# Performance work log

Measured on AMD Instinct MI355X. Metric: run time of the kernel, lower is better.

Reference implementation:

```python
import jax, jax.numpy as jnp
import numpy as np

HEAD_DIM = 128
ROPE_THETA = 10000.0


def _rope_cos_sin(positions, head_dim, theta):
    # positions: [T] int -> cos/sin [T, head_dim] (LLaMA half-split convention)
    inv_freq = 1.0 / (theta ** (jnp.arange(0, head_dim, 2, dtype=jnp.float32) / head_dim))
    ang = positions.astype(jnp.float32)[:, None] * inv_freq  # [T, D/2]
    cos = jnp.concatenate([jnp.cos(ang), jnp.cos(ang)], axis=-1)
    sin = jnp.concatenate([jnp.sin(ang), jnp.sin(ang)], axis=-1)
    return cos, sin


def _apply_rope(x, cos, sin):
    # x: [T, H, D]; rotate_half: (-x2, x1)
    half = x.shape[-1] // 2
    rot = jnp.concatenate([-x[..., half:], x[..., :half]], axis=-1)
    return x * cos[:, None, :] + rot * sin[:, None, :]


def setup_inputs() -> dict:
    key = jax.random.key(0)
    ks = jax.random.split(key, 5)
    T, hid = 4096, 4096
    S = 1024  # equal-length sequences -> B = T // S = 4
    Hq, Hk, D = 32, 8, HEAD_DIM
    hidden = jax.random.normal(ks[0], (T, hid), dtype=jnp.float32)
    positions = (jnp.arange(T, dtype=jnp.int32) % S)
    q_w = jax.random.normal(ks[1], (Hq * D, hid), dtype=jnp.float32) * 0.02
    k_w = jax.random.normal(ks[2], (Hk * D, hid), dtype=jnp.float32) * 0.02
    v_w = jax.random.normal(ks[3], (Hk * D, hid), dtype=jnp.float32) * 0.02
    o_w = jax.random.normal(ks[4], (hid, Hq * D), dtype=jnp.float32) * 0.02
    return {"hidden": hidden, "positions": positions, "q_w": q_w, "k_w": k_w,
            "v_w": v_w, "o_w": o_w, "seq_len": S}


def reference(hidden, positions, q_w, k_w, v_w, o_w, seq_len):
    T, hid = hidden.shape
    D = HEAD_DIM
    Hq = q_w.shape[0] // D
    Hk = k_w.shape[0] // D
    G = Hq // Hk  # num_kv_groups
    S = int(seq_len)
    B = T // S
    # QKV projections (ColumnParallel, tp=1): y = x @ W^T
    q = (hidden @ q_w.T).reshape(T, Hq, D)
    k = (hidden @ k_w.T).reshape(T, Hk, D)
    v = (hidden @ v_w.T).reshape(T, Hk, D)
    # fused RoPE on q and k
    cos, sin = _rope_cos_sin(positions, D, ROPE_THETA)
    q = _apply_rope(q, cos, sin)
    k = _apply_rope(k, cos, sin)
    # varlen (equal-length) causal GQA attention
    q = q.reshape(B, S, Hk, G, D)
    k = k.reshape(B, S, Hk, D)
    v = v.reshape(B, S, Hk, D)
    scale = 1.0 / np.sqrt(D).astype(np.float32)
    scores = jnp.einsum('bqhgd,bkhd->bhgqk', q, k) * scale  # [B,Hk,G,S,S]
    causal = jnp.tril(jnp.ones((S, S), dtype=bool))
    scores = jnp.where(causal, scores, jnp.asarray(-1e30, scores.dtype))
    attn = jax.nn.softmax(scores, axis=-1)
    out = jnp.einsum('bhgqk,bkhd->bqhgd', attn, v).reshape(T, Hq * D)
    # output projection (RowParallel, tp=1)
    return out @ o_w.T
```

## Files before the change

kernel.cpp:

```cpp
#include <hip/hip_runtime.h>
#include <hip/hip_bf16.h>

typedef __attribute__((ext_vector_type(8))) short bf16x8;
typedef __attribute__((ext_vector_type(4))) float f32x4;
typedef __attribute__((ext_vector_type(8))) unsigned short u16x8;

__device__ inline unsigned short f2bf(float f) {
  unsigned u = __builtin_bit_cast(unsigned, f);
  u += 0x7FFFu + ((u >> 16) & 1u);
  return (unsigned short)(u >> 16);
}
__device__ inline float b2f(unsigned short h) {
  unsigned u = ((unsigned)h) << 16;
  return __builtin_bit_cast(float, u);
}

typedef const __attribute__((address_space(1))) void* gas_ptr;
typedef __attribute__((address_space(3))) void* las_ptr;
__device__ inline void load_lds16(const void* g, void* l) {
  __builtin_amdgcn_global_load_lds((gas_ptr)g, (las_ptr)l, 16, 0, 0);
}

__global__ __launch_bounds__(256) void cvt_f32_bf16(const float* __restrict__ src,
                                                    unsigned short* __restrict__ dst,
                                                    int n4) {
  int i = blockIdx.x * 256 + threadIdx.x;
  if (i >= n4) return;
  float4 v = ((const float4*)src)[i];
  ushort4 o;
  o.x = f2bf(v.x); o.y = f2bf(v.y); o.z = f2bf(v.z); o.w = f2bf(v.w);
  ((ushort4*)dst)[i] = o;
}

template <int NLOADS>
__device__ inline void stage_tile(const unsigned short* __restrict__ g, int ld,
                                  size_t grow0, int kcol0, char* ldsdst, int tid) {
#pragma unroll
  for (int i = 0; i < NLOADS; ++i) {
    int c = tid + i * 512;
    int r = c >> 3;
    int k = (c & 7) ^ (r & 7);
    load_lds16(g + (grow0 + r) * ld + kcol0 + k * 8, ldsdst + c * 16);
  }
}

__device__ inline void xcd_decode(int orig, int nTM, int nTN, int& bm, int& bn) {
  int x = orig & 7, i = orig >> 3;
  int xr = x >> 1, xc = x & 1;
  int bmch = nTM >> 2, bnch = nTN >> 1;
  bm = xr * bmch + i / bnch;
  bn = xc * bnch + i % bnch;
}

template <int Kc, int Nc, int Mc, bool OUT_F32, bool FUSE_ROPE>
__global__ __launch_bounds__(512, 1) void gemmP(const unsigned short* __restrict__ A,
                                                const unsigned short* __restrict__ B,
                                                void* __restrict__ Cv,
                                                const int* __restrict__ positions) {
  __shared__ __attribute__((aligned(16))) char lds[147456];
  const int tid = threadIdx.x;
  const int wave = tid >> 6, lane = tid & 63;
  const int l15 = lane & 15, l4 = lane >> 4;
  const int wr = wave >> 2, wc = wave & 3;
  const int hc = wc >> 1, sb = (wc & 1) << 5;
  int bm, bn;
  xcd_decode(blockIdx.x, Mc >> 7, Nc >> 8, bm, bn);
  const size_t rowA0 = (size_t)bm << 7, rowB0 = (size_t)bn << 8;
  const int nt = Kc >> 6;

  stage_tile<2>(A, Kc, rowA0, 0,  lds + 0,             tid);
  stage_tile<4>(B, Kc, rowB0, 0,  lds + 16384,         tid);
  stage_tile<2>(A, Kc, rowA0, 64, lds + 49152,         tid);
  stage_tile<4>(B, Kc, rowB0, 64, lds + 49152 + 16384, tid);
  asm volatile("s_waitcnt vmcnt(6)" ::: "memory");
  __builtin_amdgcn_s_barrier();

  f32x4 acc[4][4] = {};

#pragma unroll 3
  for (int t = 0; t < nt; ++t) {
    const char* bufA = lds + (t % 3) * 49152;
    const char* bufB = bufA + 16384;
    char* sbuf = lds + ((t + 2) % 3) * 49152;
    const int kc2 = (t + 2) << 6;

    if (t < nt - 2) {
      stage_tile<4>(B, Kc, rowB0, kc2, sbuf + 16384, tid);
      stage_tile<2>(A, Kc, rowA0, kc2, sbuf, tid);
    }

    bf16x8 af[4][2], bf[4][2];
#pragma unroll
    for (int m = 0; m < 4; ++m) {
      int row = wr * 64 + m * 16 + l15;
#pragma unroll
      for (int kk = 0; kk < 2; ++kk)
        af[m][kk] = *(const bf16x8*)(bufA + (row << 7) + (((kk * 4 + l4) ^ (row & 7)) << 4));
    }
#pragma unroll
    for (int n = 0; n < 4; ++n) {
      int row = hc * 128 + sb + (n & 1) * 16 + ((n >> 1) << 6) + l15;
#pragma unroll
      for (int kk = 0; kk < 2; ++kk)
        bf[n][kk] = *(const bf16x8*)(bufB + (row << 7) + (((kk * 4 + l4) ^ (row & 7)) << 4));
    }

#pragma unroll
    for (int m = 0; m < 4; ++m)
#pragma unroll
      for (int n = 0; n < 4; ++n)
#pragma unroll
        for (int kk = 0; kk < 2; ++kk)
          acc[m][n] = __builtin_amdgcn_mfma_f32_16x16x32_bf16(af[m][kk], bf[n][kk], acc[m][n], 0, 0, 0);

    if (t <= nt - 3) { asm volatile("s_waitcnt vmcnt(6)" ::: "memory"); }
    else             { asm volatile("s_waitcnt vmcnt(0)" ::: "memory"); }
    asm volatile("" ::: "memory");
    __builtin_amdgcn_s_barrier();
    asm volatile("" ::: "memory");
  }

  if (FUSE_ROPE && bn < 20) {
    float invf[2];
#pragma unroll
    for (int n = 0; n < 2; ++n) {
      int d = sb + n * 16 + l15;
      invf[n] = exp2f(-(float)d * 0.20762050593046007f);
    }
#pragma unroll
    for (int m = 0; m < 4; ++m)
#pragma unroll
      for (int r = 0; r < 4; ++r) {
        int row = (int)rowA0 + wr * 64 + m * 16 + l4 * 4 + r;
        float pos = (float)positions[row];
#pragma unroll
        for (int n = 0; n < 2; ++n) {
          float s, c;
          __sincosf(pos * invf[n], &s, &c);
          float x1 = acc[m][n][r], x2 = acc[m][n + 2][r];
          acc[m][n][r]     = x1 * c - x2 * s;
          acc[m][n + 2][r] = x2 * c + x1 * s;
        }
      }
  }

#pragma unroll
  for (int m = 0; m < 4; ++m)
#pragma unroll
    for (int n = 0; n < 4; ++n)
#pragma unroll
      for (int r = 0; r < 4; ++r) {
        size_t row = rowA0 + wr * 64 + m * 16 + l4 * 4 + r;
        size_t col = rowB0 + hc * 128 + sb + (n & 1) * 16 + ((n >> 1) << 6) + l15;
        float v = acc[m][n][r];
        if (OUT_F32) ((float*)Cv)[row * Nc + col] = v;
        else         ((unsigned short*)Cv)[row * Nc + col] = f2bf(v);
      }
}

template <int Kc, int Nc, int Mc, bool OUT_F32>
__global__ __launch_bounds__(512, 1) void gemmO(const unsigned short* __restrict__ A,
                                                const unsigned short* __restrict__ B,
                                                void* __restrict__ Cv) {
  __shared__ __attribute__((aligned(16))) char lds[131072];
  const int tid = threadIdx.x;
  const int wave = tid >> 6, lane = tid & 63;
  const int l15 = lane & 15, l4 = lane >> 4;
  const int wr = wave >> 1, wc = wave & 1;
  int bm, bn;
  xcd_decode(blockIdx.x, Mc >> 8, Nc >> 8, bm, bn);
  const size_t rowA0 = (size_t)bm << 8, rowB0 = (size_t)bn << 8;
  const int nt = Kc >> 6;

  stage_tile<4>(A, Kc, rowA0, 0, lds + 0,     tid);
  stage_tile<4>(B, Kc, rowB0, 0, lds + 32768, tid);
  asm volatile("s_waitcnt vmcnt(0)" ::: "memory");
  __builtin_amdgcn_s_barrier();

  f32x4 acc[4][8] = {};

#pragma unroll 2
  for (int t = 0; t < nt; ++t) {
    const char* cbuf = lds + (t & 1) * 65536;
    char* obuf = lds + ((t + 1) & 1) * 65536;
    const char* bufA = cbuf;
    const char* bufB = cbuf + 32768;

    if (t < nt - 1) {
      stage_tile<4>(A, Kc, rowA0, (t + 1) << 6, obuf,         tid);
      stage_tile<4>(B, Kc, rowB0, (t + 1) << 6, obuf + 32768, tid);
    }

    bf16x8 af[4][2], bf[4][2];
#pragma unroll
    for (int m = 0; m < 4; ++m) {
      int row = wr * 64 + m * 16 + l15;
#pragma unroll
      for (int kk = 0; kk < 2; ++kk)
        af[m][kk] = *(const bf16x8*)(bufA + (row << 7) + (((kk * 4 + l4) ^ (row & 7)) << 4));
    }
#pragma unroll
    for (int n = 0; n < 4; ++n) {
      int row = wc * 128 + n * 16 + l15;
#pragma unroll
      for (int kk = 0; kk < 2; ++kk)
        bf[n][kk] = *(const bf16x8*)(bufB + (row << 7) + (((kk * 4 + l4) ^ (row & 7)) << 4));
    }
#pragma unroll
    for (int m = 0; m < 4; ++m)
#pragma unroll
      for (int n = 0; n < 4; ++n)
#pragma unroll
        for (int kk = 0; kk < 2; ++kk)
          acc[m][n] = __builtin_amdgcn_mfma_f32_16x16x32_bf16(af[m][kk], bf[n][kk], acc[m][n], 0, 0, 0);
#pragma unroll
    for (int n = 0; n < 4; ++n) {
      int row = wc * 128 + (n + 4) * 16 + l15;
#pragma unroll
      for (int kk = 0; kk < 2; ++kk)
        bf[n][kk] = *(const bf16x8*)(bufB + (row << 7) + (((kk * 4 + l4) ^ (row & 7)) << 4));
    }
#pragma unroll
    for (int m = 0; m < 4; ++m)
#pragma unroll
      for (int n = 0; n < 4; ++n)
#pragma unroll
        for (int kk = 0; kk < 2; ++kk)
          acc[m][n + 4] = __builtin_amdgcn_mfma_f32_16x16x32_bf16(af[m][kk], bf[n][kk], acc[m][n + 4], 0, 0, 0);

    asm volatile("s_waitcnt vmcnt(0)" ::: "memory");
    asm volatile("" ::: "memory");
    __builtin_amdgcn_s_barrier();
    asm volatile("" ::: "memory");
  }

#pragma unroll
  for (int m = 0; m < 4; ++m)
#pragma unroll
    for (int n = 0; n < 8; ++n)
#pragma unroll
      for (int r = 0; r < 4; ++r) {
        size_t row = rowA0 + wr * 64 + m * 16 + l4 * 4 + r;
        size_t col = rowB0 + wc * 128 + n * 16 + l15;
        float v = acc[m][n][r];
        if (OUT_F32) ((float*)Cv)[row * Nc + col] = v;
        else         ((unsigned short*)Cv)[row * Nc + col] = f2bf(v);
      }
}

__global__ __launch_bounds__(256, 4) void attn_kernel(const unsigned short* __restrict__ qkv,
                                                      unsigned short* __restrict__ ao) {
  int orig = blockIdx.x;
  int wgid = (orig & 7) * 128 + (orig >> 3);
  int pair = wgid & 7;
  int hq = (wgid >> 3) & 31;
  int b  = wgid >> 8;
  int hk = hq >> 2;
  int tid = threadIdx.x, wave = tid >> 6, lane = tid & 63;
  int l15 = lane & 15, l4 = lane >> 4;

  __shared__ __attribute__((aligned(16))) char ldsA[16384];
  __shared__ __attribute__((aligned(16))) unsigned short Vt[128][72];
  unsigned short (*Ks)[128]    = (unsigned short (*)[128])ldsA;
  unsigned short (*Ps)[16][72] = (unsigned short (*)[16][72])ldsA;

  const float scale = 0.08838834764831845f;

#pragma unroll 1
  for (int iq = 0; iq < 2; ++iq) {
    const int qa = iq ? (15 - pair) : pair;
    const size_t qrow0 = (size_t)(b * 1024 + qa * 64 + wave * 16);

    bf16x8 qf[4];
    {
      const unsigned short* qp = qkv + (qrow0 + l15) * 6144 + ((size_t)hq << 7) + l4 * 8;
#pragma unroll
      for (int kc = 0; kc < 4; ++kc) qf[kc] = *(const bf16x8*)(qp + kc * 32);
    }

    float m_i[4], l_i[4];
    f32x4 oacc[8];
#pragma unroll
    for (int r = 0; r < 4; ++r) { m_i[r] = -1e30f; l_i[r] = 0.0f; }
#pragma unroll
    for (int d = 0; d < 8; ++d) oacc[d] = f32x4{0.f, 0.f, 0.f, 0.f};

#pragma unroll 1
    for (int kt = 0; kt <= qa; ++kt) {
      __syncthreads();

      const unsigned short* kbase = qkv + (size_t)(b * 1024 + kt * 64) * 6144 + 4096 + ((size_t)hk << 7);
#pragma unroll
      for (int j = 0; j < 4; ++j) {
        int c = (j * 4 + wave) * 64 + lane;
        int r = c >> 4;
        int cc = (c & 15) ^ (r & 7);
        load_lds16(kbase + (size_t)r * 6144 + cc * 8, ldsA + c * 16);
      }
      {
        const unsigned short* vp = qkv + (size_t)(b * 1024 + kt * 64 + lane) * 6144 + 5120 + ((size_t)hk << 7) + wave * 32;
        u16x8 va0 = *(const u16x8*)(vp);
        u16x8 va1 = *(const u16x8*)(vp + 8);
        u16x8 va2 = *(const u16x8*)(vp + 16);
        u16x8 va3 = *(const u16x8*)(vp + 24);
        int d0 = wave * 32;
#pragma unroll
        for (int c = 0; c < 8; ++c) Vt[d0 + c][lane]      = va0[c];
#pragma unroll
        for (int c = 0; c < 8; ++c) Vt[d0 + 8 + c][lane]  = va1[c];
#pragma unroll
        for (int c = 0; c < 8; ++c) Vt[d0 + 16 + c][lane] = va2[c];
#pragma unroll
        for (int c = 0; c < 8; ++c) Vt[d0 + 24 + c][lane] = va3[c];
      }
      __syncthreads();

      float pbuf[4][4];
      float tmax[4] = {-1e30f, -1e30f, -1e30f, -1e30f};
#pragma unroll
      for (int nt = 0; nt < 4; ++nt) {
        f32x4 sacc = {0.f, 0.f, 0.f, 0.f};
        int row = nt * 16 + l15;
#pragma unroll
        for (int kc = 0; kc < 4; ++kc) {
          const unsigned short* kp = &Ks[0][0] + row * 128 + (((kc * 4 + l4) ^ (row & 7)) * 8);
          bf16x8 kf = *(const bf16x8*)kp;
          sacc = __builtin_amdgcn_mfma_f32_16x16x32_bf16(qf[kc], kf, sacc, 0, 0, 0);
        }
#pragma unroll
        for (int r = 0; r < 4; ++r) {
          float s = sacc[r] * scale;
          if (kt == qa) {
            int kcol = nt * 16 + l15;
            int qrow = wave * 16 + l4 * 4 + r;
            if (kcol > qrow) s = -1e30f;
          }
          pbuf[nt][r] = s;
          tmax[r] = fmaxf(tmax[r], s);
        }
      }
      __syncthreads();

#pragma unroll
      for (int r = 0; r < 4; ++r) {
        float v = tmax[r];
        v = fmaxf(v, __shfl_xor(v, 1));
        v = fmaxf(v, __shfl_xor(v, 2));
        v = fmaxf(v, __shfl_xor(v, 4));
        v = fmaxf(v, __shfl_xor(v, 8));
        tmax[r] = v;
      }
      float rescale[4];
#pragma unroll
      for (int r = 0; r < 4; ++r) {
        float mn = fmaxf(m_i[r], tmax[r]);
        rescale[r] = __expf(m_i[r] - mn);
        m_i[r] = mn;
      }
      float psum[4] = {0.f, 0.f, 0.f, 0.f};
#pragma unroll
      for (int nt = 0; nt < 4; ++nt)
#pragma unroll
        for (int r = 0; r < 4; ++r) {
          float p = __expf(pbuf[nt][r] - m_i[r]);
          pbuf[nt][r] = p;
          psum[r] += p;
        }
#pragma unroll
      for (int r = 0; r < 4; ++r) {
        float v = psum[r];
        v += __shfl_xor(v, 1);
        v += __shfl_xor(v, 2);
        v += __shfl_xor(v, 4);
        v += __shfl_xor(v, 8);
        l_i[r] = l_i[r] * rescale[r] + v;
      }
#pragma unroll
      for (int d = 0; d < 8; ++d)
#pragma unroll
        for (int r = 0; r < 4; ++r) oacc[d][r] *= rescale[r];

#pragma unroll
      for (int nt = 0; nt < 4; ++nt)
#pragma unroll
        for (int r = 0; r < 4; ++r)
          Ps[wave][l4 * 4 + r][nt * 16 + l15] = f2bf(pbuf[nt][r]);

#pragma unroll
      for (int h = 0; h < 2; ++h) {
        bf16x8 pa = *(const bf16x8*)&Ps[wave][l15][h * 32 + l4 * 8];
#pragma unroll
        for (int d = 0; d < 8; ++d) {
          bf16x8 vf = *(const bf16x8*)&Vt[d * 16 + l15][h * 32 + l4 * 8];
          oacc[d] = __builtin_amdgcn_mfma_f32_16x16x32_bf16(pa, vf, oacc[d], 0, 0, 0);
        }
      }
    }

#pragma unroll
    for (int d = 0; d < 8; ++d)
#pragma unroll
      for (int r = 0; r < 4; ++r) {
        size_t row = qrow0 + l4 * 4 + r;
        size_t col = ((size_t)hq << 7) + d * 16 + l15;
        ao[row * 4096 + col] = f2bf(oacc[d][r] / l_i[r]);
      }
  }
}

extern "C" void kernel_launch(void* const* d_in, const int* in_sizes, int n_in,
                              void* d_out, int out_size, void* d_ws, size_t ws_size,
                              hipStream_t stream) {
  const float* hidden    = (const float*)d_in[0];
  const int*   positions = (const int*)d_in[1];
  const float* q_w       = (const float*)d_in[2];
  const float* k_w       = (const float*)d_in[3];
  const float* v_w       = (const float*)d_in[4];
  const float* o_w       = (const float*)d_in[5];
  float* out = (float*)d_out;

  char* ws = (char*)d_ws;
  unsigned short* hidB  = (unsigned short*)(ws);
  unsigned short* wqkvB = (unsigned short*)(ws + 33554432);
  unsigned short* woB   = (unsigned short*)(ws + 83886080);
  unsigned short* qkvB  = (unsigned short*)(ws + 117440512);
  unsigned short* aoB   = (unsigned short*)(ws + 167772160);

  cvt_f32_bf16<<<16384, 256, 0, stream>>>(hidden, hidB, 4194304);
  cvt_f32_bf16<<<16384, 256, 0, stream>>>(q_w, wqkvB, 4194304);
  cvt_f32_bf16<<<4096, 256, 0, stream>>>(k_w, wqkvB + 16777216, 1048576);
  cvt_f32_bf16<<<4096, 256, 0, stream>>>(v_w, wqkvB + 20971520, 1048576);
  cvt_f32_bf16<<<16384, 256, 0, stream>>>(o_w, woB, 4194304);

  gemmP<4096, 6144, 4096, false, true><<<768, 512, 0, stream>>>(hidB, wqkvB, (void*)qkvB, positions);

  attn_kernel<<<1024, 256, 0, stream>>>(qkvB, aoB);

  gemmO<4096, 4096, 4096, true><<<256, 512, 0, stream>>>(aoB, woB, (void*)out);
}
```

Baseline: 476.2 us.

## Double-buffer K/V tiles in attention kernel to overlap loads with compute

The attention kernel now keeps two LDS buffers for K and transposed V and gives P its own buffer instead of aliasing it over K. While the current tile is processed, the next tile's K is fetched asynchronously and its V is held in registers, then written to LDS after the PV MFMAs. This cuts the barriers per iteration from three to one and hides global load latency. In exchange it uses more LDS and registers, and launch bounds drop from 4 to 2 waves per SIMD, which lowers occupancy.

```diff
diff --git a/kernel.cpp b/kernel.cpp
--- a/kernel.cpp
+++ b/kernel.cpp
@@ -248,7 +248,7 @@
       }
 }
 
-__global__ __launch_bounds__(256, 4) void attn_kernel(const unsigned short* __restrict__ qkv,
+__global__ __launch_bounds__(256, 2) void attn_kernel(const unsigned short* __restrict__ qkv,
                                                       unsigned short* __restrict__ ao) {
   int orig = blockIdx.x;
   int wgid = (orig & 7) * 128 + (orig >> 3);
@@ -259,12 +259,12 @@
   int tid = threadIdx.x, wave = tid >> 6, lane = tid & 63;
   int l15 = lane & 15, l4 = lane >> 4;
 
-  __shared__ __attribute__((aligned(16))) char ldsA[16384];
-  __shared__ __attribute__((aligned(16))) unsigned short Vt[128][72];
-  unsigned short (*Ks)[128]    = (unsigned short (*)[128])ldsA;
-  unsigned short (*Ps)[16][72] = (unsigned short (*)[16][72])ldsA;
+  __shared__ __attribute__((aligned(16))) unsigned short Ks[2][64][128];
+  __shared__ __attribute__((aligned(16))) unsigned short Vt[2][128][72];
+  __shared__ __attribute__((aligned(16))) unsigned short Ps[4][16][72];
 
   const float scale = 0.08838834764831845f;
+  const size_t kvrow0 = (size_t)(b * 1024);
 
 #pragma unroll 1
   for (int iq = 0; iq < 2; ++iq) {
@@ -285,35 +285,54 @@
 #pragma unroll
     for (int d = 0; d < 8; ++d) oacc[d] = f32x4{0.f, 0.f, 0.f, 0.f};
 
-#pragma unroll 1
-    for (int kt = 0; kt <= qa; ++kt) {
-      __syncthreads();
-
-      const unsigned short* kbase = qkv + (size_t)(b * 1024 + kt * 64) * 6144 + 4096 + ((size_t)hk << 7);
+    {
+      const unsigned short* kbase = qkv + kvrow0 * 6144 + 4096 + ((size_t)hk << 7);
 #pragma unroll
       for (int j = 0; j < 4; ++j) {
         int c = (j * 4 + wave) * 64 + lane;
         int r = c >> 4;
         int cc = (c & 15) ^ (r & 7);
-        load_lds16(kbase + (size_t)r * 6144 + cc * 8, ldsA + c * 16);
-      }
-      {
-        const unsigned short* vp = qkv + (size_t)(b * 1024 + kt * 64 + lane) * 6144 + 5120 + ((size_t)hk << 7) + wave * 32;
-        u16x8 va0 = *(const u16x8*)(vp);
-        u16x8 va1 = *(const u16x8*)(vp + 8);
-        u16x8 va2 = *(const u16x8*)(vp + 16);
-        u16x8 va3 = *(const u16x8*)(vp + 24);
-        int d0 = wave * 32;
-#pragma unroll
-        for (int c = 0; c < 8; ++c) Vt[d0 + c][lane]      = va0[c];
-#pragma unroll
-        for (int c = 0; c < 8; ++c) Vt[d0 + 8 + c][lane]  = va1[c];
-#pragma unroll
-        for (int c = 0; c < 8; ++c) Vt[d0 + 16 + c][lane] = va2[c];
-#pragma unroll
-        for (int c = 0; c < 8; ++c) Vt[d0 + 24 + c][lane] = va3[c];
-      }
-      __syncthreads();
+        load_lds16(kbase + (size_t)r * 6144 + cc * 8, (char*)&Ks[0][0][0] + c * 16);
+      }
+      const unsigned short* vp = qkv + (kvrow0 + lane) * 6144 + 5120 + ((size_t)hk << 7) + wave * 32;
+      u16x8 va0 = *(const u16x8*)(vp);
+      u16x8 va1 = *(const u16x8*)(vp + 8);
+      u16x8 va2 = *(const u16x8*)(vp + 16);
+      u16x8 va3 = *(const u16x8*)(vp + 24);
+      int d0 = wave * 32;
+#pragma unroll
+      for (int c = 0; c < 8; ++c) Vt[0][d0 + c][lane]      = va0[c];
+#pragma unroll
+      for (int c = 0; c < 8; ++c) Vt[0][d0 + 8 + c][lane]  = va1[c];
+#pragma unroll
+      for (int c = 0; c < 8; ++c) Vt[0][d0 + 16 + c][lane] = va2[c];
+#pragma unroll
+      for (int c = 0; c < 8; ++c) Vt[0][d0 + 24 + c][lane] = va3[c];
+      asm volatile("s_waitcnt vmcnt(0) lgkmcnt(0)" ::: "memory");
+      __builtin_amdgcn_s_barrier();
+    }
+
+#pragma unroll 1
+    for (int kt = 0; kt <= qa; ++kt) {
+      const int cur = kt & 1, nxt = cur ^ 1;
+      const bool more = (kt < qa);
+
+      u16x8 va0, va1, va2, va3;
+      if (more) {
+        const unsigned short* kbase = qkv + (kvrow0 + (kt + 1) * 64) * 6144 + 4096 + ((size_t)hk << 7);
+#pragma unroll
+        for (int j = 0; j < 4; ++j) {
+          int c = (j * 4 + wave) * 64 + lane;
+          int r = c >> 4;
+          int cc = (c & 15) ^ (r & 7);
+          load_lds16(kbase + (size_t)r * 6144 + cc * 8, (char*)&Ks[nxt][0][0] + c * 16);
+        }
+        const unsigned short* vp = qkv + (kvrow0 + (kt + 1) * 64 + lane) * 6144 + 5120 + ((size_t)hk << 7) + wave * 32;
+        va0 = *(const u16x8*)(vp);
+        va1 = *(const u16x8*)(vp + 8);
+        va2 = *(const u16x8*)(vp + 16);
+        va3 = *(const u16x8*)(vp + 24);
+      }
 
       float pbuf[4][4];
       float tmax[4] = {-1e30f, -1e30f, -1e30f, -1e30f};
@@ -323,7 +342,7 @@
         int row = nt * 16 + l15;
 #pragma unroll
         for (int kc = 0; kc < 4; ++kc) {
-          const unsigned short* kp = &Ks[0][0] + row * 128 + (((kc * 4 + l4) ^ (row & 7)) * 8);
+          const unsigned short* kp = &Ks[cur][0][0] + row * 128 + (((kc * 4 + l4) ^ (row & 7)) * 8);
           bf16x8 kf = *(const bf16x8*)kp;
           sacc = __builtin_amdgcn_mfma_f32_16x16x32_bf16(qf[kc], kf, sacc, 0, 0, 0);
         }
@@ -339,7 +358,6 @@
           tmax[r] = fmaxf(tmax[r], s);
         }
       }
-      __syncthreads();
 
 #pragma unroll
       for (int r = 0; r < 4; ++r) {
@@ -391,10 +409,26 @@
         bf16x8 pa = *(const bf16x8*)&Ps[wave][l15][h * 32 + l4 * 8];
 #pragma unroll
         for (int d = 0; d < 8; ++d) {
-          bf16x8 vf = *(const bf16x8*)&Vt[d * 16 + l15][h * 32 + l4 * 8];
+          bf16x8 vf = *(const bf16x8*)&Vt[cur][d * 16 + l15][h * 32 + l4 * 8];
           oacc[d] = __builtin_amdgcn_mfma_f32_16x16x32_bf16(pa, vf, oacc[d], 0, 0, 0);
         }
       }
+
+      if (more) {
+        int d0 = wave * 32;
+#pragma unroll
+        for (int c = 0; c < 8; ++c) Vt[nxt][d0 + c][lane]      = va0[c];
+#pragma unroll
+        for (int c = 0; c < 8; ++c) Vt[nxt][d0 + 8 + c][lane]  = va1[c];
+#pragma unroll
+        for (int c = 0; c < 8; ++c) Vt[nxt][d0 + 16 + c][lane] = va2[c];
+#pragma unroll
+        for (int c = 0; c < 8; ++c) Vt[nxt][d0 + 24 + c][lane] = va3[c];
+      }
+
+      asm volatile("s_waitcnt vmcnt(0) lgkmcnt(0)" ::: "memory");
+      __builtin_amdgcn_s_barrier();
+      asm volatile("" ::: "memory");
     }
 
 #pragma unroll
```

Result: no change. 476.1 us (-0.0%).

## Enlarge attention query tile to 128 rows with 8 waves sharing K/V tiles

Applied to the files above, without the earlier changes.

Attention blocks now hold 8 waves covering 128 query rows instead of 4 waves covering 64. Each K/V tile loaded into LDS is shared by twice as many query rows, and the grid is halved. The P buffer gets its own LDS region so one barrier per iteration can be dropped. Waves whose rows lie fully above the causal diagonal skip compute on the last tile, and the mask is recomputed per wave. The cost is more LDS per block, fewer resident blocks, and idle waves on diagonal tiles.

```diff
diff --git a/kernel.cpp b/kernel.cpp
--- a/kernel.cpp
+++ b/kernel.cpp
@@ -248,28 +248,28 @@
       }
 }
 
-__global__ __launch_bounds__(256, 4) void attn_kernel(const unsigned short* __restrict__ qkv,
+__global__ __launch_bounds__(512, 2) void attn_kernel(const unsigned short* __restrict__ qkv,
                                                       unsigned short* __restrict__ ao) {
   int orig = blockIdx.x;
-  int wgid = (orig & 7) * 128 + (orig >> 3);
-  int pair = wgid & 7;
-  int hq = (wgid >> 3) & 31;
-  int b  = wgid >> 8;
+  int wgid = (orig & 7) * 64 + (orig >> 3);
+  int pair = wgid & 3;
+  int hq = (wgid >> 2) & 31;
+  int b  = wgid >> 7;
   int hk = hq >> 2;
   int tid = threadIdx.x, wave = tid >> 6, lane = tid & 63;
   int l15 = lane & 15, l4 = lane >> 4;
 
-  __shared__ __attribute__((aligned(16))) char ldsA[16384];
+  __shared__ __attribute__((aligned(16))) unsigned short Ks[64][128];
   __shared__ __attribute__((aligned(16))) unsigned short Vt[128][72];
-  unsigned short (*Ks)[128]    = (unsigned short (*)[128])ldsA;
-  unsigned short (*Ps)[16][72] = (unsigned short (*)[16][72])ldsA;
+  __shared__ __attribute__((aligned(16))) unsigned short Ps[8][16][72];
 
   const float scale = 0.08838834764831845f;
 
 #pragma unroll 1
   for (int iq = 0; iq < 2; ++iq) {
-    const int qa = iq ? (15 - pair) : pair;
-    const size_t qrow0 = (size_t)(b * 1024 + qa * 64 + wave * 16);
+    const int qa = iq ? (7 - pair) : pair;
+    const int qbase = qa * 128 + wave * 16;
+    const size_t qrow0 = (size_t)(b * 1024 + qbase);
 
     bf16x8 qf[4];
     {
@@ -285,35 +285,34 @@
 #pragma unroll
     for (int d = 0; d < 8; ++d) oacc[d] = f32x4{0.f, 0.f, 0.f, 0.f};
 
+    const int nkt = 2 * qa + 2;
+
 #pragma unroll 1
-    for (int kt = 0; kt <= qa; ++kt) {
+    for (int kt = 0; kt < nkt; ++kt) {
       __syncthreads();
 
       const unsigned short* kbase = qkv + (size_t)(b * 1024 + kt * 64) * 6144 + 4096 + ((size_t)hk << 7);
 #pragma unroll
-      for (int j = 0; j < 4; ++j) {
-        int c = (j * 4 + wave) * 64 + lane;
+      for (int j = 0; j < 2; ++j) {
+        int c = tid + j * 512;
         int r = c >> 4;
         int cc = (c & 15) ^ (r & 7);
-        load_lds16(kbase + (size_t)r * 6144 + cc * 8, ldsA + c * 16);
+        load_lds16(kbase + (size_t)r * 6144 + cc * 8, (char*)&Ks[0][0] + c * 16);
       }
       {
-        const unsigned short* vp = qkv + (size_t)(b * 1024 + kt * 64 + lane) * 6144 + 5120 + ((size_t)hk << 7) + wave * 32;
+        const unsigned short* vp = qkv + (size_t)(b * 1024 + kt * 64 + lane) * 6144 + 5120 + ((size_t)hk << 7) + wave * 16;
         u16x8 va0 = *(const u16x8*)(vp);
         u16x8 va1 = *(const u16x8*)(vp + 8);
-        u16x8 va2 = *(const u16x8*)(vp + 16);
-        u16x8 va3 = *(const u16x8*)(vp + 24);
-        int d0 = wave * 32;
-#pragma unroll
-        for (int c = 0; c < 8; ++c) Vt[d0 + c][lane]      = va0[c];
-#pragma unroll
-        for (int c = 0; c < 8; ++c) Vt[d0 + 8 + c][lane]  = va1[c];
-#pragma unroll
-        for (int c = 0; c < 8; ++c) Vt[d0 + 16 + c][lane] = va2[c];
-#pragma unroll
-        for (int c = 0; c < 8; ++c) Vt[d0 + 24 + c][lane] = va3[c];
+        int d0 = wave * 16;
+#pragma unroll
+        for (int c = 0; c < 8; ++c) Vt[d0 + c][lane]     = va0[c];
+#pragma unroll
+        for (int c = 0; c < 8; ++c) Vt[d0 + 8 + c][lane] = va1[c];
       }
       __syncthreads();
+
+      if (kt * 64 > qbase + 15) continue;
+      const bool partial = (kt * 64 + 63 > qbase);
 
       float pbuf[4][4];
       float tmax[4] = {-1e30f, -1e30f, -1e30f, -1e30f};
@@ -330,16 +329,15 @@
 #pragma unroll
         for (int r = 0; r < 4; ++r) {
           float s = sacc[r] * scale;
-          if (kt == qa) {
-            int kcol = nt * 16 + l15;
-            int qrow = wave * 16 + l4 * 4 + r;
+          if (partial) {
+            int kcol = kt * 64 + nt * 16 + l15;
+            int qrow = qbase + l4 * 4 + r;
             if (kcol > qrow) s = -1e30f;
           }
           pbuf[nt][r] = s;
           tmax[r] = fmaxf(tmax[r], s);
         }
       }
-      __syncthreads();
 
 #pragma unroll
       for (int r = 0; r < 4; ++r) {
@@ -434,7 +432,7 @@
 
   gemmP<4096, 6144, 4096, false, true><<<768, 512, 0, stream>>>(hidB, wqkvB, (void*)qkvB, positions);
 
-  attn_kernel<<<1024, 256, 0, stream>>>(qkvB, aoB);
+  attn_kernel<<<512, 512, 0, stream>>>(qkvB, aoB);
 
   gemmO<4096, 4096, 4096, true><<<256, 512, 0, stream>>>(aoB, woB, (void*)out);
 }
```

Result: no change. 479.4 us (+0.7%).
